# Kernel tuning notes

Measured on AMD Instinct MI355X. Metric: run time of the kernel, lower is better.

## Reference

```python
import jax, jax.numpy as jnp
import numpy as np
from jax import lax

KH = KW = 3
STRIDE = (1, 1)
PAD = (1, 1)

def setup_inputs() -> dict:
    key = jax.random.key(0)
    k1, k2, k3 = jax.random.split(key, 3)
    B_, C, H, W = 16, 128, 56, 56
    O, R = 256, 16
    Kflat = C * KH * KW
    x = jax.random.normal(k1, (B_, C, H, W), dtype=jnp.float32)
    # kaiming_normal_ fan_out for A: std = sqrt(2/out_channels)
    A = jax.random.normal(k2, (O, R), dtype=jnp.float32) * np.float32(np.sqrt(2.0 / O))
    # kaiming_normal_ fan_in for B: std = sqrt(2/kernel_flat_dim)
    Bm = jax.random.normal(k3, (R, Kflat), dtype=jnp.float32) * np.float32(np.sqrt(2.0 / Kflat))
    return {"x": x, "A": A, "B": Bm}

def reference(x, A, B):
    b, c, h, w = x.shape
    h_out = (h + 2 * PAD[0] - KH) // STRIDE[0] + 1
    w_out = (w + 2 * PAD[1] - KW) // STRIDE[1] + 1
    # im2col: [B, C*KH*KW, H_out, W_out]; feature order (c, kh, kw) matches torch Unfold
    patches = lax.conv_general_dilated_patches(
        x, filter_shape=(KH, KW), window_strides=STRIDE,
        padding=((PAD[0], PAD[0]), (PAD[1], PAD[1])))
    patches = patches.reshape(b, c * KH * KW, h_out * w_out)  # [B, K, L]
    tmp = jnp.einsum('rk,bkl->brl', B, patches)               # rank-limited matmul
    out = jnp.einsum('or,brl->bol', A, tmp)                   # [B, O, L]
    return out.reshape(b, A.shape[0], h_out, w_out)
```

## Files before the change

### kernel.cpp

```cpp
#include <hip/hip_runtime.h>
#include <hip/hip_bf16.h>


#define Bn 16
#define Cc 128
#define Hh 56
#define Ww 56
#define Ll (Hh * Ww)
#define Rr 16
#define Oo 256
#define KF (Cc * 9)
#define HB 2

__device__ __forceinline__ float bf16_bits(unsigned short u) {
    return __uint_as_float(((unsigned)u) << 16);
}

template<bool BF>
__device__ __forceinline__ float ld(const void* __restrict__ p, unsigned i) {
    if constexpr (BF) return bf16_bits(((const unsigned short*)p)[i]);
    else              return ((const float*)p)[i];
}

__device__ __forceinline__ bool detect_bf16(const void* __restrict__ p) {
    const unsigned* w = (const unsigned*)p;
    int c = 0;
#pragma unroll
    for (int i = 0; i < 32; ++i) {
        const unsigned e = (w[i] >> 7) & 0xFFu;
        c += (e >= 96u && e <= 144u) ? 1 : 0;
    }
    return c >= 20;
}

__global__ __launch_bounds__(256) void prep_kernel(
    const void* __restrict__ A, const void* __restrict__ Bm,
    float* __restrict__ Bt, float* __restrict__ Afp)
{
    const bool ab = detect_bf16(A);
    const bool bb = detect_bf16(Bm);
    const int i = blockIdx.x * 256 + threadIdx.x;
    if (i < KF * Rr) {
        const int k = i >> 4, r = i & 15;
        Bt[i] = bb ? bf16_bits(((const unsigned short*)Bm)[r * KF + k])
                   : ((const float*)Bm)[r * KF + k];
    }
    if (i < Oo * Rr) {
        Afp[i] = ab ? bf16_bits(((const unsigned short*)A)[i])
                    : ((const float*)A)[i];
    }
}

#define CONV_BODY(CC, XBUF)                                                  \
    {                                                                        \
        float xv[HB + 2];                                                    \
        _Pragma("unroll")                                                    \
        for (int rr = 0; rr < HB + 2; ++rr) xv[rr] = XBUF[rr];               \
        const int ccn = ((CC) + 4 < 32) ? (CC) + 4 : (CC);                   \
        const unsigned coffn = (unsigned)(ccn * Ll);                         \
        _Pragma("unroll")                                                    \
        for (int rr = 0; rr < HB + 2; ++rr) {                                \
            const float v = ld<XB>(x, rowb[rr] + coffn);                     \
            XBUF[rr] = hv[rr] ? v : 0.f;                                     \
        }                                                                    \
        const float* bt = btb + (size_t)((CC) * 9) * Rr;                     \
        _Pragma("unroll")                                                    \
        for (int dh = 0; dh < 3; ++dh) {                                     \
            const float x0 = xv[dh];                                         \
            const float x1 = xv[dh + 1];                                     \
            _Pragma("unroll")                                                \
            for (int dw = 0; dw < 3; ++dw) {                                 \
                const float* bp = bt + (dh * 3 + dw) * Rr;                   \
                _Pragma("unroll")                                            \
                for (int j = 0; j < 8; ++j) {                                \
                    const float bv = bp[j];              \
                    a[0][dw][j] += bv * x0;                                  \
                    a[1][dw][j] += bv * x1;                                  \
                }                                                            \
            }                                                                \
        }                                                                    \
    }

template<bool XB>
__device__ __forceinline__ void main_body(
    const void* __restrict__ x,
    const float* __restrict__ Bt,
    const float* __restrict__ Afp,
    float* __restrict__ out,
    float (* __restrict__ part)[4][Rr][64],
    float (* __restrict__ tmp2)[64][17])
{
    const int tid  = threadIdx.x;
    const int lane = tid & 63;
    const int wv   = __builtin_amdgcn_readfirstlane(tid >> 6);
    const int cs   = wv & 3;
    const int rh   = wv >> 2;
    const int h0   = blockIdx.x * HB;
    const int b    = blockIdx.y;
    const int w    = lane;
    const bool wok = (w < Ww);
    const int  wcl = wok ? w : (Ww - 1);

    float a[HB][3][8];
#pragma unroll
    for (int row = 0; row < HB; ++row)
#pragma unroll
        for (int dw = 0; dw < 3; ++dw)
#pragma unroll
            for (int j = 0; j < 8; ++j) a[row][dw][j] = 0.f;

    const unsigned xbase = (unsigned)(b * Cc * Ll + (cs * 32) * Ll);
    const float* btb = Bt + (size_t)(cs * 32 * 9) * Rr + rh * 8;

    unsigned rowb[HB + 2];
    bool     hv[HB + 2];
#pragma unroll
    for (int rr = 0; rr < HB + 2; ++rr) {
        const int hh  = h0 - 1 + rr;
        hv[rr] = (hh >= 0) & (hh < Hh);
        const int hcl = hv[rr] ? hh : (hh < 0 ? 0 : Hh - 1);
        rowb[rr] = xbase + (unsigned)(hcl * Ww) + (unsigned)wcl;
    }

    float xb0[HB + 2], xb1[HB + 2], xb2[HB + 2], xb3[HB + 2];
#pragma unroll
    for (int rr = 0; rr < HB + 2; ++rr) {
        const float v0 = ld<XB>(x, rowb[rr]);
        xb0[rr] = hv[rr] ? v0 : 0.f;
        const float v1 = ld<XB>(x, rowb[rr] + (unsigned)Ll);
        xb1[rr] = hv[rr] ? v1 : 0.f;
        const float v2 = ld<XB>(x, rowb[rr] + (unsigned)(2 * Ll));
        xb2[rr] = hv[rr] ? v2 : 0.f;
        const float v3 = ld<XB>(x, rowb[rr] + (unsigned)(3 * Ll));
        xb3[rr] = hv[rr] ? v3 : 0.f;
    }
    for (int t = 0; t < 8; ++t) {
        CONV_BODY(4 * t,     xb0)
        CONV_BODY(4 * t + 1, xb1)
        CONV_BODY(4 * t + 2, xb2)
        CONV_BODY(4 * t + 3, xb3)
    }

#pragma unroll
    for (int row = 0; row < HB; ++row)
#pragma unroll
    for (int j = 0; j < 8; ++j) {
        const float up = __shfl(a[row][0][j], w - 1);
        const float dn = __shfl(a[row][2][j], w + 1);
        float s = a[row][1][j];
        s += (w > 0)      ? up : 0.f;
        s += (w < Ww - 1) ? dn : 0.f;
        part[row][cs][rh * 8 + j][lane] = s;
    }
    __syncthreads();

    {
        const int px = tid & 63;
        const int rr = (tid >> 6) & 7;
#pragma unroll
        for (int row = 0; row < HB; ++row)
#pragma unroll
        for (int t = 0; t < 2; ++t) {
            const int r = rr + t * 8;
            tmp2[row][px][r] = part[row][0][r][px] + part[row][1][r][px]
                             + part[row][2][r][px] + part[row][3][r][px];
        }
    }
    __syncthreads();

    float tv[HB][Rr];
#pragma unroll
    for (int row = 0; row < HB; ++row)
#pragma unroll
        for (int r = 0; r < Rr; ++r) tv[row][r] = tmp2[row][lane][r];

    const size_t obase = (size_t)b * Oo * Ll + (size_t)(h0 * Ww) + (size_t)w;
#pragma unroll 4
    for (int j = 0; j < 32; ++j) {
        const int o = wv * 32 + j;
        const float* Ao = Afp + (size_t)o * Rr;
        float s0 = 0.f, s1 = 0.f;
#pragma unroll
        for (int r = 0; r < Rr; ++r) {
            const float av = Ao[r];
            s0 += av * tv[0][r];
            s1 += av * tv[1][r];
        }
        if (wok) {
            __builtin_nontemporal_store(s0, &out[obase + (size_t)o * Ll]);
            __builtin_nontemporal_store(s1, &out[obase + (size_t)o * Ll + Ww]);
        }
    }
}

__global__ __launch_bounds__(512, 4) void fused_big(
    const void* __restrict__ x,
    const float* __restrict__ Bt,
    const float* __restrict__ Afp,
    float* __restrict__ out)
{
    __shared__ float part[HB][4][Rr][64];
    __shared__ float tmp2[HB][64][17];
    if (detect_bf16(x)) main_body<true >(x, Bt, Afp, out, part, tmp2);
    else                main_body<false>(x, Bt, Afp, out, part, tmp2);
}

__global__ __launch_bounds__(256) void fused_fallback(
    const void* __restrict__ x, const void* __restrict__ A,
    const void* __restrict__ Bm, float* __restrict__ out)
{
    const bool xb = detect_bf16(x);
    const bool ab = detect_bf16(A);
    const bool bb = detect_bf16(Bm);
    const int gid = blockIdx.x * 256 + threadIdx.x;
    const int b = gid / Ll;
    const int l = gid - b * Ll;
    const int h = l / Ww, w = l - h * Ww;
    float acc[Rr];
#pragma unroll
    for (int r = 0; r < Rr; ++r) acc[r] = 0.f;
    const size_t xbase = (size_t)b * Cc * Ll;
    for (int c = 0; c < Cc; ++c) {
        const size_t xc = xbase + (size_t)c * Ll;
        float xv[9];
#pragma unroll
        for (int dh = 0; dh < 3; ++dh) {
            const int hh = h + dh - 1;
            const bool hok = (hh >= 0) & (hh < Hh);
#pragma unroll
            for (int dw = 0; dw < 3; ++dw) {
                const int ww = w + dw - 1;
                const bool ok = hok & (ww >= 0) & (ww < Ww);
                const size_t idx = xc + (size_t)(hh * Ww + ww);
                xv[dh*3+dw] = ok ? (xb ? bf16_bits(((const unsigned short*)x)[idx])
                                       : ((const float*)x)[idx]) : 0.f;
            }
        }
#pragma unroll
        for (int r = 0; r < Rr; ++r) {
            const size_t bo = (size_t)r * KF + (size_t)c * 9;
            float s = acc[r];
#pragma unroll
            for (int i = 0; i < 9; ++i)
                s += (bb ? bf16_bits(((const unsigned short*)Bm)[bo+i])
                         : ((const float*)Bm)[bo+i]) * xv[i];
            acc[r] = s;
        }
    }
    const size_t obase = (size_t)b * Oo * Ll + (size_t)l;
    for (int o = 0; o < Oo; ++o) {
        float s = 0.f;
#pragma unroll
        for (int r = 0; r < Rr; ++r)
            s += (ab ? bf16_bits(((const unsigned short*)A)[o*Rr+r])
                     : ((const float*)A)[o*Rr+r]) * acc[r];
        out[obase + (size_t)o * Ll] = s;
    }
}

extern "C" void kernel_launch(void* const* d_in, const int* in_sizes, int n_in,
                              void* d_out, int out_size, void* d_ws, size_t ws_size,
                              hipStream_t stream) {
    const void* x  = d_in[0];
    const void* A  = d_in[1];
    const void* Bm = d_in[2];
    for (int i = 0; i < n_in && i < 3; ++i) {
        const int s = in_sizes[i];
        if      (s == Bn * Cc * Ll) x  = d_in[i];
        else if (s == Oo * Rr)      A  = d_in[i];
        else if (s == Rr * KF)      Bm = d_in[i];
    }
    float* out = (float*)d_out;

    const size_t need = (size_t)(KF * Rr + Oo * Rr) * sizeof(float);
    if (ws_size >= need) {
        float* Bt  = (float*)d_ws;
        float* Afp = Bt + KF * Rr;
        prep_kernel<<<dim3((KF * Rr + 255) / 256), 256, 0, stream>>>(A, Bm, Bt, Afp);
        fused_big<<<dim3(Hh / HB, Bn), 512, 0, stream>>>(x, Bt, Afp, out);
    } else {
        fused_fallback<<<dim3((Bn * Ll) / 256), 256, 0, stream>>>(x, A, Bm, out);
    }
}
```

Measured before the change: 117.8 us.

## Use bf16 MFMA implicit GEMM with NHWC padded input and split-precision weights

Adds a new default path with three steps. First, a pre-pass transposes x into a zero-padded NHWC bf16 buffer. Second, B is packed into MFMA fragment order as hi/lo bf16 pairs. Third, the rank-16 projection over all 9 taps and 128 channels runs as 16x16x32 bf16 MFMAs per 16-pixel tile, then A is applied in fp32 from shared memory. This replaces the scalar FMA convolution loop with matrix-core work, at the cost of an extra transpose kernel, about 13 MB of workspace, and rounding x to bf16, which may loosen accuracy.

```diff
diff --git a/kernel.cpp b/kernel.cpp
--- a/kernel.cpp
+++ b/kernel.cpp
@@ -10,10 +10,22 @@
 #define Rr 16
 #define Oo 256
 #define KF (Cc * 9)
+#define NKS 36
+#define H2 (Hh + 2)
+#define W2 (Ww + 2)
 #define HB 2
+
+typedef __attribute__((ext_vector_type(8))) short bfrag_t;
+typedef __attribute__((ext_vector_type(4))) float f32x4;
 
 __device__ __forceinline__ float bf16_bits(unsigned short u) {
     return __uint_as_float(((unsigned)u) << 16);
+}
+
+__device__ __forceinline__ unsigned short bf16_rne(float f) {
+    const unsigned u = __float_as_uint(f);
+    const unsigned r = u + 0x7FFFu + ((u >> 16) & 1u);
+    return (unsigned short)(r >> 16);
 }
 
 template<bool BF>
@@ -33,7 +45,136 @@
     return c >= 20;
 }
 
-__global__ __launch_bounds__(256) void prep_kernel(
+__global__ __launch_bounds__(256) void prep_frag(
+    const void* __restrict__ A, const void* __restrict__ Bm,
+    unsigned short* __restrict__ Bfrag, float* __restrict__ Afp)
+{
+    const bool ab = detect_bf16(A);
+    const bool bb = detect_bf16(Bm);
+    const int i = blockIdx.x * 256 + threadIdx.x;
+    if (i < NKS * 512) {
+        const int kstep = i >> 9, rem = i & 511;
+        const int l = rem >> 3, e = rem & 7;
+        const int r = l & 15, g = l >> 4;
+        const int kp = kstep * 32 + g * 8 + e;
+        const int tap = kp >> 7, c = kp & 127;
+        const int k = c * 9 + tap;
+        const float v = bb ? bf16_bits(((const unsigned short*)Bm)[r * KF + k])
+                           : ((const float*)Bm)[r * KF + k];
+        const unsigned short hi = bf16_rne(v);
+        const float lov = v - bf16_bits(hi);
+        Bfrag[(kstep * 2 + 0) * 512 + rem] = hi;
+        Bfrag[(kstep * 2 + 1) * 512 + rem] = bf16_rne(lov);
+    }
+    if (i < Oo * Rr) {
+        Afp[i] = ab ? bf16_bits(((const unsigned short*)A)[i])
+                    : ((const float*)A)[i];
+    }
+}
+
+__global__ __launch_bounds__(256) void transpose_x(
+    const void* __restrict__ x, unsigned short* __restrict__ xt)
+{
+    __shared__ unsigned short tile[Cc][Ww + 1];
+    const bool xb = detect_bf16(x);
+    const int tid = threadIdx.x;
+    const int h2  = blockIdx.x;
+    const int b   = blockIdx.y;
+    const unsigned rowbase = (unsigned)(((b * H2 + h2) * W2) * Cc);
+    unsigned* xtw = (unsigned*)xt;
+    if (h2 == 0 || h2 == H2 - 1) {
+        for (int i = tid; i < W2 * Cc / 2; i += 256)
+            xtw[rowbase / 2 + i] = 0u;
+        return;
+    }
+    const int h = h2 - 1;
+    const unsigned xrow = (unsigned)(b * Cc * Ll + h * Ww);
+#pragma unroll 4
+    for (int it = 0; it < 32; ++it) {
+        const int i = it * 256 + tid;
+        const int c = i >> 6, wl = i & 63;
+        if (wl < Ww) {
+            unsigned short v;
+            if (xb) v = ((const unsigned short*)x)[xrow + (unsigned)c * Ll + (unsigned)wl];
+            else    v = bf16_rne(((const float*)x)[xrow + (unsigned)c * Ll + (unsigned)wl]);
+            tile[c][wl] = v;
+        }
+    }
+    __syncthreads();
+#pragma unroll 4
+    for (int it = 0; it < 28; ++it) {
+        const int j = it * 256 + tid;
+        const int c = j & 127, w = j >> 7;
+        xt[rowbase + (unsigned)((w + 1) * Cc + c)] = tile[c][w];
+    }
+    if (tid < 64)
+        xtw[rowbase / 2 + tid] = 0u;
+    else if (tid < 128)
+        xtw[(rowbase + (unsigned)((W2 - 1) * Cc)) / 2 + (tid - 64)] = 0u;
+}
+
+__global__ __launch_bounds__(256, 4) void fused_mfma2(
+    const unsigned short* __restrict__ xt,
+    const unsigned short* __restrict__ Bfrag,
+    const float* __restrict__ Afp,
+    float* __restrict__ out)
+{
+    __shared__ float tmp[Rr][66];
+    const int tid  = threadIdx.x;
+    const int lane = tid & 63;
+    const int wv   = __builtin_amdgcn_readfirstlane(tid >> 6);
+    const int col  = lane & 15;
+    const int g    = lane >> 4;
+    const int h    = blockIdx.x;
+    const int b    = blockIdx.y;
+    const int px   = wv * 16 + col;
+    const int pxc  = px < Ww ? px : Ww - 1;
+
+    unsigned tb[9];
+#pragma unroll
+    for (int dh = 0; dh < 3; ++dh)
+#pragma unroll
+        for (int dw = 0; dw < 3; ++dw)
+            tb[dh * 3 + dw] =
+                (unsigned)(((b * H2 + h + dh) * W2 + pxc + dw) * Cc);
+
+    f32x4 acc = {0.f, 0.f, 0.f, 0.f};
+    const bfrag_t* __restrict__ bf = (const bfrag_t*)Bfrag;
+    const unsigned ge = (unsigned)(g * 8);
+
+#pragma unroll
+    for (int ks = 0; ks < NKS; ++ks) {
+        const int tap = ks >> 2, cb = ks & 3;
+        const bfrag_t pf = *(const bfrag_t*)(xt + tb[tap] + (unsigned)(cb * 32) + ge);
+        const bfrag_t ahi = bf[(ks * 2 + 0) * 64 + lane];
+        const bfrag_t alo = bf[(ks * 2 + 1) * 64 + lane];
+        acc = __builtin_amdgcn_mfma_f32_16x16x32_bf16(ahi, pf, acc, 0, 0, 0);
+        acc = __builtin_amdgcn_mfma_f32_16x16x32_bf16(alo, pf, acc, 0, 0, 0);
+    }
+
+#pragma unroll
+    for (int reg = 0; reg < 4; ++reg)
+        tmp[g * 4 + reg][wv * 16 + col] = acc[reg];
+    __syncthreads();
+
+    float tv[Rr];
+#pragma unroll
+    for (int r = 0; r < Rr; ++r) tv[r] = tmp[r][lane];
+
+    const bool wok = (lane < Ww);
+    const size_t obase = (size_t)b * Oo * Ll + (size_t)(h * Ww) + (size_t)lane;
+#pragma unroll 4
+    for (int j = 0; j < 64; ++j) {
+        const int o = wv * 64 + j;
+        const float* Ao = Afp + (size_t)o * Rr;
+        float s = 0.f;
+#pragma unroll
+        for (int r = 0; r < Rr; ++r) s += Ao[r] * tv[r];
+        if (wok) out[obase + (size_t)o * Ll] = s;
+    }
+}
+
+__global__ __launch_bounds__(256) void prep_flat(
     const void* __restrict__ A, const void* __restrict__ Bm,
     float* __restrict__ Bt, float* __restrict__ Afp)
 {
@@ -73,7 +214,7 @@
                 const float* bp = bt + (dh * 3 + dw) * Rr;                   \
                 _Pragma("unroll")                                            \
                 for (int j = 0; j < 8; ++j) {                                \
-                    const float bv = bp[j];              \
+                    const float bv = bp[j];                                  \
                     a[0][dw][j] += bv * x0;                                  \
                     a[1][dw][j] += bv * x1;                                  \
                 }                                                            \
@@ -82,7 +223,7 @@
     }
 
 template<bool XB>
-__device__ __forceinline__ void main_body(
+__device__ __forceinline__ void mid_body(
     const void* __restrict__ x,
     const float* __restrict__ Bt,
     const float* __restrict__ Afp,
@@ -153,7 +294,6 @@
         part[row][cs][rh * 8 + j][lane] = s;
     }
     __syncthreads();
-
     {
         const int px = tid & 63;
         const int rr = (tid >> 6) & 7;
@@ -187,13 +327,13 @@
             s1 += av * tv[1][r];
         }
         if (wok) {
-            __builtin_nontemporal_store(s0, &out[obase + (size_t)o * Ll]);
-            __builtin_nontemporal_store(s1, &out[obase + (size_t)o * Ll + Ww]);
-        }
-    }
-}
-
-__global__ __launch_bounds__(512, 4) void fused_big(
+            out[obase + (size_t)o * Ll]      = s0;
+            out[obase + (size_t)o * Ll + Ww] = s1;
+        }
+    }
+}
+
+__global__ __launch_bounds__(512, 4) void fused_mid(
     const void* __restrict__ x,
     const float* __restrict__ Bt,
     const float* __restrict__ Afp,
@@ -201,8 +341,8 @@
 {
     __shared__ float part[HB][4][Rr][64];
     __shared__ float tmp2[HB][64][17];
-    if (detect_bf16(x)) main_body<true >(x, Bt, Afp, out, part, tmp2);
-    else                main_body<false>(x, Bt, Afp, out, part, tmp2);
+    if (detect_bf16(x)) mid_body<true >(x, Bt, Afp, out, part, tmp2);
+    else                mid_body<false>(x, Bt, Afp, out, part, tmp2);
 }
 
 __global__ __launch_bounds__(256) void fused_fallback(
@@ -272,12 +412,24 @@
     }
     float* out = (float*)d_out;
 
-    const size_t need = (size_t)(KF * Rr + Oo * Rr) * sizeof(float);
-    if (ws_size >= need) {
+    const size_t frag_bytes = (size_t)(NKS * 2 * 512) * 2;
+    const size_t afp_bytes  = (size_t)(Oo * Rr) * 4;
+    const size_t xt_bytes   = (size_t)Bn * H2 * W2 * Cc * 2;
+    const size_t need_big   = frag_bytes + afp_bytes + xt_bytes;
+    const size_t need_mid   = frag_bytes + afp_bytes;
+
+    if (ws_size >= need_big) {
+        unsigned short* Bfrag = (unsigned short*)d_ws;
+        float* Afp = (float*)((char*)d_ws + frag_bytes);
+        unsigned short* xt = (unsigned short*)((char*)d_ws + frag_bytes + afp_bytes);
+        prep_frag<<<dim3(72), 256, 0, stream>>>(A, Bm, Bfrag, Afp);
+        transpose_x<<<dim3(H2, Bn), 256, 0, stream>>>(x, xt);
+        fused_mfma2<<<dim3(Hh, Bn), 256, 0, stream>>>(xt, Bfrag, Afp, out);
+    } else if (ws_size >= need_mid) {
         float* Bt  = (float*)d_ws;
         float* Afp = Bt + KF * Rr;
-        prep_kernel<<<dim3((KF * Rr + 255) / 256), 256, 0, stream>>>(A, Bm, Bt, Afp);
-        fused_big<<<dim3(Hh / HB, Bn), 512, 0, stream>>>(x, Bt, Afp, out);
+        prep_flat<<<dim3((KF * Rr + 255) / 256), 256, 0, stream>>>(A, Bm, Bt, Afp);
+        fused_mid<<<dim3(Hh / HB, Bn), 512, 0, stream>>>(x, Bt, Afp, out);
     } else {
         fused_fallback<<<dim3((Bn * Ll) / 256), 256, 0, stream>>>(x, A, Bm, out);
     }
```

New measurement: 137.5 us. 16.8% more time.
